# Performance work log

Measured on AMD Instinct MI355X. Metric: run time of the kernel, lower is better.

Reference implementation:

```python
import jax, jax.numpy as jnp
import numpy as np

D_MODEL = 1024
N_HEADS = 16
HEAD_DIM = D_MODEL // N_HEADS


def setup_inputs() -> dict:
    key = jax.random.key(0)
    ks = jax.random.split(key, 9)
    s = 1.0 / np.sqrt(D_MODEL)
    inp = {
        "x": jax.random.normal(ks[0], (4, 2048, D_MODEL), dtype=jnp.float32),
        "wq": jax.random.uniform(ks[1], (D_MODEL, D_MODEL), jnp.float32, -s, s),
        "bq": jax.random.uniform(ks[2], (D_MODEL,), jnp.float32, -s, s),
        "wk": jax.random.uniform(ks[3], (D_MODEL, D_MODEL), jnp.float32, -s, s),
        "bk": jax.random.uniform(ks[4], (D_MODEL,), jnp.float32, -s, s),
        "wv": jax.random.uniform(ks[5], (D_MODEL, D_MODEL), jnp.float32, -s, s),
        "bv": jax.random.uniform(ks[6], (D_MODEL,), jnp.float32, -s, s),
        "wo": jax.random.uniform(ks[7], (D_MODEL, D_MODEL), jnp.float32, -s, s),
        "bo": jax.random.uniform(ks[8], (D_MODEL,), jnp.float32, -s, s),
    }
    return inp


def reference(x, wq, bq, wk, bk, wv, bv, wo, bo):
    b, s, d = x.shape
    h, hd = N_HEADS, HEAD_DIM
    # projections (torch Linear: y = x @ W.T + b; here weights stored as [in, out])
    q = (x @ wq + bq).reshape(b, s, h, hd).transpose(0, 2, 1, 3)  # [b,h,s,hd]
    k = (x @ wk + bk).reshape(b, s, h, hd).transpose(0, 2, 1, 3)
    v = (x @ wv + bv).reshape(b, s, h, hd).transpose(0, 2, 1, 3)
    scores = jnp.einsum("bhqd,bhkd->bhqk", q, k) / jnp.sqrt(jnp.float32(hd))
    causal = jnp.tril(jnp.ones((s, s), dtype=bool))
    scores = jnp.where(causal, scores, -jnp.inf)
    weights = jax.nn.softmax(scores, axis=-1)
    attn = jnp.einsum("bhqk,bhkd->bhqd", weights, v)  # [b,h,s,hd]
    attn = attn.transpose(0, 2, 1, 3).reshape(b, s, d)
    return attn @ wo + bo
```

## Files before the change

kernel.cpp:

```cpp
#include <hip/hip_runtime.h>
#include <cstddef>

#define D_MODEL 1024
#define NH 16
#define HD 64
#define BATCH 4
#define SEQ 2048
#define MTOT (BATCH * SEQ)

typedef _Float16 half8 __attribute__((ext_vector_type(8)));
typedef _Float16 half4v __attribute__((ext_vector_type(4)));
typedef float f32x4 __attribute__((ext_vector_type(4)));

#if __has_builtin(__builtin_amdgcn_exp2f)
#define EXP2(x) __builtin_amdgcn_exp2f(x)
#else
#define EXP2(x) __expf((x)*0.69314718056f)
#endif

__global__ __launch_bounds__(256) void prep(
    const float* __restrict__ x, _Float16* __restrict__ xh,
    const float* __restrict__ W0, const float* __restrict__ W1,
    const float* __restrict__ W2, const float* __restrict__ W3,
    _Float16* __restrict__ T0, _Float16* __restrict__ T1,
    _Float16* __restrict__ T2, _Float16* __restrict__ T3)
{
    __shared__ float T[64][65];
    const int bid = blockIdx.x;
    if (bid < 256) {
        const size_t base = (size_t)bid * 4096 + threadIdx.x;
#pragma unroll
        for (int it = 0; it < 16; ++it) {
            const size_t i = base + (size_t)it * 256;
            const float4* p = (const float4*)x + 2 * i;
            float4 a = p[0], b = p[1];
            half8 h;
            h[0] = (_Float16)a.x; h[1] = (_Float16)a.y; h[2] = (_Float16)a.z; h[3] = (_Float16)a.w;
            h[4] = (_Float16)b.x; h[5] = (_Float16)b.y; h[6] = (_Float16)b.z; h[7] = (_Float16)b.w;
            *((half8*)xh + i) = h;
        }
    } else {
        const int t = bid - 256;
        const int mtx = t >> 8;
        const float* W = (mtx == 0) ? W0 : (mtx == 1) ? W1 : (mtx == 2) ? W2 : W3;
        _Float16*   Wt = (mtx == 0) ? T0 : (mtx == 1) ? T1 : (mtx == 2) ? T2 : T3;
        const int tile = t & 255;
        const int k0 = (tile >> 4) * 64, n0 = (tile & 15) * 64;
        const int r = threadIdx.x >> 4, c4 = (threadIdx.x & 15) * 4;

#pragma unroll
        for (int i = 0; i < 4; ++i) {
            float4 v = *(const float4*)(W + (size_t)(k0 + r + 16 * i) * 1024 + n0 + c4);
            T[r + 16 * i][c4 + 0] = v.x; T[r + 16 * i][c4 + 1] = v.y;
            T[r + 16 * i][c4 + 2] = v.z; T[r + 16 * i][c4 + 3] = v.w;
        }
        __syncthreads();
#pragma unroll
        for (int i = 0; i < 4; ++i) {
            const int n = r + 16 * i;
            half4v h;
            h[0] = (_Float16)T[c4 + 0][n]; h[1] = (_Float16)T[c4 + 1][n];
            h[2] = (_Float16)T[c4 + 2][n]; h[3] = (_Float16)T[c4 + 3][n];
            *(half4v*)(Wt + (size_t)(n0 + n) * 1024 + k0 + c4) = h;
        }
    }
}

template <int QKV>
__global__ __launch_bounds__(256) void gemm_mfma(
    const _Float16* __restrict__ A,
    const _Float16* __restrict__ Bt0, const _Float16* __restrict__ Bt1, const _Float16* __restrict__ Bt2,
    const float* __restrict__ bi0, const float* __restrict__ bi1, const float* __restrict__ bi2,
    void* __restrict__ C0, void* __restrict__ C1, void* __restrict__ C2)
{
    const int L = blockIdx.x;
    const int y = L & 63;
    const int c_ = L >> 6;
    const int z  = QKV ? (c_ >> 3) : 0;
    const int xb = QKV ? (c_ & 7) : c_;

    const _Float16* Bt = (z == 0) ? Bt0 : (z == 1) ? Bt1 : Bt2;
    const float*   bia = (z == 0) ? bi0 : (z == 1) ? bi1 : bi2;
    void*            C = (z == 0) ? C0  : (z == 1) ? C1  : C2;

    __shared__ _Float16 As[128][72];
    __shared__ _Float16 Bs[128][72];

    const int tid  = threadIdx.x;
    const int w    = tid >> 6;
    const int lane = tid & 63;
    const int l15  = lane & 15;
    const int lg   = lane >> 4;
    const int m0 = y * 128;
    const int n0 = xb * 128;
    const int wm = (w >> 1) * 64, wn = (w & 1) * 64;

    const int srow = tid >> 3;
    const int scol = (tid & 7) * 8;

    const _Float16* Ab = A + (size_t)(m0 + srow) * 1024 + scol;
    const _Float16* Bb = Bt + (size_t)(n0 + srow) * 1024 + scol;

    half8 aR[4], bR[4];
#pragma unroll
    for (int i = 0; i < 4; ++i) {
        aR[i] = *(const half8*)(Ab + (size_t)(32 * i) * 1024);
        bR[i] = *(const half8*)(Bb + (size_t)(32 * i) * 1024);
    }

    f32x4 acc[4][4];
#pragma unroll
    for (int i = 0; i < 4; ++i)
#pragma unroll
        for (int j = 0; j < 4; ++j) { acc[i][j][0] = 0.f; acc[i][j][1] = 0.f; acc[i][j][2] = 0.f; acc[i][j][3] = 0.f; }

    for (int kt = 0; kt < 16; ++kt) {
        __syncthreads();
#pragma unroll
        for (int i = 0; i < 4; ++i) {
            *(half8*)&As[srow + 32 * i][scol] = aR[i];
            *(half8*)&Bs[srow + 32 * i][scol] = bR[i];
        }
        __syncthreads();
        if (kt < 15) {
            const int k0 = (kt + 1) * 64;
#pragma unroll
            for (int i = 0; i < 4; ++i) {
                aR[i] = *(const half8*)(Ab + (size_t)(32 * i) * 1024 + k0);
                bR[i] = *(const half8*)(Bb + (size_t)(32 * i) * 1024 + k0);
            }
        }
#pragma unroll
        for (int c = 0; c < 2; ++c) {
            half8 af[4], bf[4];
#pragma unroll
            for (int i = 0; i < 4; ++i) af[i] = *(const half8*)&As[wm + 16 * i + l15][32 * c + 8 * lg];
#pragma unroll
            for (int j = 0; j < 4; ++j) bf[j] = *(const half8*)&Bs[wn + 16 * j + l15][32 * c + 8 * lg];
#pragma unroll
            for (int i = 0; i < 4; ++i)
#pragma unroll
                for (int j = 0; j < 4; ++j)
                    acc[i][j] = __builtin_amdgcn_mfma_f32_16x16x32_f16(af[i], bf[j], acc[i][j], 0, 0, 0);
        }
    }

    float bv[4];
#pragma unroll
    for (int j = 0; j < 4; ++j) bv[j] = bia[n0 + wn + 16 * j + l15];

#pragma unroll
    for (int i = 0; i < 4; ++i)
#pragma unroll
        for (int j = 0; j < 4; ++j)
#pragma unroll
            for (int r = 0; r < 4; ++r) {
                const int m = m0 + wm + 16 * i + 4 * lg + r;
                const int n = n0 + wn + 16 * j + l15;
                const float val = acc[i][j][r] + bv[j];
                if (QKV) {
                    const int bb = m >> 11, ss = m & 2047, hh = n >> 6, hd = n & 63;
                    if (z < 2)
                        ((_Float16*)C)[((size_t)(bb * NH + hh) * SEQ + ss) * HD + hd] = (_Float16)val;
                    else
                        ((_Float16*)C)[((size_t)(bb * NH + hh) * HD + hd) * SEQ + ss] = (_Float16)val;
                } else {
                    ((float*)C)[(size_t)m * 1024 + n] = val;
                }
            }
}

__global__ __launch_bounds__(256, 4) void attn_fwd_mfma(
    const _Float16* __restrict__ Q, const _Float16* __restrict__ K,
    const _Float16* __restrict__ Vt, _Float16* __restrict__ O)
{
    __shared__ _Float16 Ks[64][80];
    __shared__ _Float16 Vs[64][80];
    __shared__ _Float16 Ps[4][16][80];

    const int tid  = threadIdx.x;
    const int w    = tid >> 6;
    const int lane = tid & 63;
    const int l15  = lane & 15;
    const int lg   = lane >> 4;

    const int bh = blockIdx.y;
    const int b  = bh >> 4, h = bh & 15;

    const _Float16* Qb  = Q  + (size_t)bh * SEQ * HD;
    const _Float16* Kb  = K  + (size_t)bh * SEQ * HD;
    const _Float16* Vtb = Vt + (size_t)bh * HD * SEQ;

    const int srow = tid >> 3;
    const int scol = (tid & 7) * 8;

    for (int pass = 0; pass < 2; ++pass) {
        const int qt = pass ? (int)blockIdx.x : (31 - (int)blockIdx.x);
        const int q0 = qt * 64;
        const int ntiles = qt + 1;

        half8 qa[2];
        {
            const _Float16* qp = Qb + (size_t)(q0 + 16 * w + l15) * HD + 8 * lg;
            qa[0] = *(const half8*)(qp);
            qa[1] = *(const half8*)(qp + 32);
#pragma unroll
            for (int c = 0; c < 2; ++c)
#pragma unroll
                for (int j = 0; j < 8; ++j)
                    qa[c][j] = (_Float16)((float)qa[c][j] * 0.18033688f);
        }

        f32x4 o_[4];
#pragma unroll
        for (int ft = 0; ft < 4; ++ft) { o_[ft][0] = 0.f; o_[ft][1] = 0.f; o_[ft][2] = 0.f; o_[ft][3] = 0.f; }
        float lp[4] = {0.f, 0.f, 0.f, 0.f};

        half8 kreg[2], vreg[2];
#pragma unroll
        for (int j = 0; j < 2; ++j) {
            kreg[j] = *(const half8*)(Kb  + (size_t)(srow + 32 * j) * HD + scol);
            vreg[j] = *(const half8*)(Vtb + (size_t)(srow + 32 * j) * SEQ + scol);
        }

        for (int kt = 0; kt < ntiles; ++kt) {
            __syncthreads();
#pragma unroll
            for (int j = 0; j < 2; ++j) {
                *(half8*)&Ks[srow + 32 * j][scol] = kreg[j];
                *(half8*)&Vs[srow + 32 * j][scol] = vreg[j];
            }
            __syncthreads();

            if (kt + 1 < ntiles) {
                const int k0 = (kt + 1) * 64;
#pragma unroll
                for (int j = 0; j < 2; ++j) {
                    kreg[j] = *(const half8*)(Kb  + (size_t)(k0 + srow + 32 * j) * HD + scol);
                    vreg[j] = *(const half8*)(Vtb + (size_t)(srow + 32 * j) * SEQ + k0 + scol);
                }
            }

            f32x4 s[4];
#pragma unroll
            for (int f = 0; f < 4; ++f) { s[f][0] = 0.f; s[f][1] = 0.f; s[f][2] = 0.f; s[f][3] = 0.f; }
#pragma unroll
            for (int c = 0; c < 2; ++c)
#pragma unroll
                for (int f = 0; f < 4; ++f) {
                    half8 kb = *(const half8*)&Ks[16 * f + l15][32 * c + 8 * lg];
                    s[f] = __builtin_amdgcn_mfma_f32_16x16x32_f16(qa[c], kb, s[f], 0, 0, 0);
                }

            const bool dg = (kt == qt);
#pragma unroll
            for (int f = 0; f < 4; ++f)
#pragma unroll
                for (int r = 0; r < 4; ++r) {
                    float p = EXP2(s[f][r]);
                    if (dg && (16 * f + l15 > 16 * w + 4 * lg + r)) p = 0.f;
                    lp[r] += p;
                    Ps[w][4 * lg + r][16 * f + l15] = (_Float16)p;
                }

            half8 pa[2];
            pa[0] = *(const half8*)&Ps[w][l15][8 * lg];
            pa[1] = *(const half8*)&Ps[w][l15][32 + 8 * lg];
#pragma unroll
            for (int c = 0; c < 2; ++c)
#pragma unroll
                for (int ft = 0; ft < 4; ++ft) {
                    half8 vb = *(const half8*)&Vs[16 * ft + l15][32 * c + 8 * lg];
                    o_[ft] = __builtin_amdgcn_mfma_f32_16x16x32_f16(pa[c], vb, o_[ft], 0, 0, 0);
                }
        }

#pragma unroll
        for (int r = 0; r < 4; ++r) {
            float rs = lp[r];
            rs += __shfl_xor(rs, 1);
            rs += __shfl_xor(rs, 2);
            rs += __shfl_xor(rs, 4);
            rs += __shfl_xor(rs, 8);
            const float inv = 1.0f / rs;
            _Float16* orow = O + (size_t)(b * SEQ + q0 + 16 * w + 4 * lg + r) * D_MODEL + h * HD + l15;
#pragma unroll
            for (int ft = 0; ft < 4; ++ft) orow[16 * ft] = (_Float16)(o_[ft][r] * inv);
        }
        __syncthreads();
    }
}

extern "C" void kernel_launch(void* const* d_in, const int* in_sizes, int n_in,
                              void* d_out, int out_size, void* d_ws, size_t ws_size,
                              hipStream_t stream)
{
    const float* x  = (const float*)d_in[0];
    const float* wq = (const float*)d_in[1];
    const float* bq = (const float*)d_in[2];
    const float* wk = (const float*)d_in[3];
    const float* bk = (const float*)d_in[4];
    const float* wv = (const float*)d_in[5];
    const float* bv = (const float*)d_in[6];
    const float* wo = (const float*)d_in[7];
    const float* bo = (const float*)d_in[8];
    float* out = (float*)d_out;

    const size_t SZ = (size_t)MTOT * D_MODEL;
    const size_t WZ = (size_t)D_MODEL * D_MODEL;

    _Float16* xh  = (_Float16*)d_ws;
    _Float16* wtq = xh + SZ;
    _Float16* wtk = wtq + WZ;
    _Float16* wtv = wtk + WZ;
    _Float16* wto = wtv + WZ;
    _Float16* Qh  = wto + WZ;
    _Float16* Kh  = Qh + SZ;
    _Float16* Vtg = Kh + SZ;
    _Float16* AOh = Vtg + SZ;

    prep<<<dim3(1280), 256, 0, stream>>>(x, xh, wq, wk, wv, wo, wtq, wtk, wtv, wto);
    gemm_mfma<1><<<dim3(1536), 256, 0, stream>>>(xh, wtq, wtk, wtv, bq, bk, bv, Qh, Kh, Vtg);
    attn_fwd_mfma<<<dim3(16, BATCH * NH), 256, 0, stream>>>(Qh, Kh, Vtg, AOh);
    gemm_mfma<0><<<dim3(512), 256, 0, stream>>>(AOh, wto, wto, wto, bo, bo, bo, out, out, out);
}
```

Measured before the change: 272.1 us.

## Load A operands directly from global memory into registers, share only B tile

```diff
diff --git a/kernel.cpp b/kernel.cpp
--- a/kernel.cpp
+++ b/kernel.cpp
@@ -66,104 +66,108 @@
     }
 }
 
-template <int QKV>
-__global__ __launch_bounds__(256) void gemm_mfma(
+template <int QKV, int BMW>
+__global__ __launch_bounds__(256, (BMW == 64) ? 3 : 4) void gemm_flat(
     const _Float16* __restrict__ A,
     const _Float16* __restrict__ Bt0, const _Float16* __restrict__ Bt1, const _Float16* __restrict__ Bt2,
     const float* __restrict__ bi0, const float* __restrict__ bi1, const float* __restrict__ bi2,
     void* __restrict__ C0, void* __restrict__ C1, void* __restrict__ C2)
 {
-    const int L = blockIdx.x;
-    const int y = L & 63;
-    const int c_ = L >> 6;
-    const int z  = QKV ? (c_ >> 3) : 0;
-    const int xb = QKV ? (c_ & 7) : c_;
+    constexpr int NI = BMW / 16;
+    constexpr int MB = QKV ? 32 : 64;
+
+    const int L  = blockIdx.x;
+    const int y  = L & (MB - 1);
+    const int c_ = L / MB;
+    const int z  = QKV ? (c_ >> 4) : 0;
+    const int xb = QKV ? (c_ & 15) : c_;
 
     const _Float16* Bt = (z == 0) ? Bt0 : (z == 1) ? Bt1 : Bt2;
     const float*   bia = (z == 0) ? bi0 : (z == 1) ? bi1 : bi2;
     void*            C = (z == 0) ? C0  : (z == 1) ? C1  : C2;
 
-    __shared__ _Float16 As[128][72];
-    __shared__ _Float16 Bs[128][72];
+    __shared__ _Float16 Bs[64][72];
 
     const int tid  = threadIdx.x;
     const int w    = tid >> 6;
     const int lane = tid & 63;
     const int l15  = lane & 15;
     const int lg   = lane >> 4;
-    const int m0 = y * 128;
-    const int n0 = xb * 128;
-    const int wm = (w >> 1) * 64, wn = (w & 1) * 64;
+    const int m0 = y * (4 * BMW);
+    const int n0 = xb * 64;
 
     const int srow = tid >> 3;
     const int scol = (tid & 7) * 8;
 
-    const _Float16* Ab = A + (size_t)(m0 + srow) * 1024 + scol;
     const _Float16* Bb = Bt + (size_t)(n0 + srow) * 1024 + scol;
-
-    half8 aR[4], bR[4];
-#pragma unroll
-    for (int i = 0; i < 4; ++i) {
-        aR[i] = *(const half8*)(Ab + (size_t)(32 * i) * 1024);
-        bR[i] = *(const half8*)(Bb + (size_t)(32 * i) * 1024);
-    }
-
-    f32x4 acc[4][4];
-#pragma unroll
-    for (int i = 0; i < 4; ++i)
+    const _Float16* Aw = A + (size_t)(m0 + w * BMW + l15) * 1024 + 8 * lg;
+
+    half8 bR[2];
+#pragma unroll
+    for (int j = 0; j < 2; ++j)
+        bR[j] = *(const half8*)(Bb + (size_t)(32 * j) * 1024);
+
+    f32x4 acc[NI][4];
+#pragma unroll
+    for (int i = 0; i < NI; ++i)
 #pragma unroll
         for (int j = 0; j < 4; ++j) { acc[i][j][0] = 0.f; acc[i][j][1] = 0.f; acc[i][j][2] = 0.f; acc[i][j][3] = 0.f; }
 
     for (int kt = 0; kt < 16; ++kt) {
+        const int k0 = kt * 64;
         __syncthreads();
 #pragma unroll
-        for (int i = 0; i < 4; ++i) {
-            *(half8*)&As[srow + 32 * i][scol] = aR[i];
-            *(half8*)&Bs[srow + 32 * i][scol] = bR[i];
-        }
+        for (int j = 0; j < 2; ++j)
+            *(half8*)&Bs[srow + 32 * j][scol] = bR[j];
         __syncthreads();
         if (kt < 15) {
-            const int k0 = (kt + 1) * 64;
-#pragma unroll
-            for (int i = 0; i < 4; ++i) {
-                aR[i] = *(const half8*)(Ab + (size_t)(32 * i) * 1024 + k0);
-                bR[i] = *(const half8*)(Bb + (size_t)(32 * i) * 1024 + k0);
-            }
-        }
-#pragma unroll
-        for (int c = 0; c < 2; ++c) {
-            half8 af[4], bf[4];
-#pragma unroll
-            for (int i = 0; i < 4; ++i) af[i] = *(const half8*)&As[wm + 16 * i + l15][32 * c + 8 * lg];
-#pragma unroll
-            for (int j = 0; j < 4; ++j) bf[j] = *(const half8*)&Bs[wn + 16 * j + l15][32 * c + 8 * lg];
-#pragma unroll
-            for (int i = 0; i < 4; ++i)
+#pragma unroll
+            for (int j = 0; j < 2; ++j)
+                bR[j] = *(const half8*)(Bb + (size_t)(32 * j) * 1024 + k0 + 64);
+        }
+
+        half8 af[NI][2];
+#pragma unroll
+        for (int i = 0; i < NI; ++i)
+#pragma unroll
+            for (int c = 0; c < 2; ++c)
+                af[i][c] = *(const half8*)(Aw + (size_t)(16 * i) * 1024 + k0 + 32 * c);
+
+        half8 bf[4][2];
+#pragma unroll
+        for (int j = 0; j < 4; ++j)
+#pragma unroll
+            for (int c = 0; c < 2; ++c)
+                bf[j][c] = *(const half8*)&Bs[16 * j + l15][32 * c + 8 * lg];
+
+#pragma unroll
+        for (int c = 0; c < 2; ++c)
+#pragma unroll
+            for (int i = 0; i < NI; ++i)
 #pragma unroll
                 for (int j = 0; j < 4; ++j)
-                    acc[i][j] = __builtin_amdgcn_mfma_f32_16x16x32_f16(af[i], bf[j], acc[i][j], 0, 0, 0);
-        }
+                    acc[i][j] = __builtin_amdgcn_mfma_f32_16x16x32_f16(af[i][c], bf[j][c], acc[i][j], 0, 0, 0);
     }
 
     float bv[4];
 #pragma unroll
-    for (int j = 0; j < 4; ++j) bv[j] = bia[n0 + wn + 16 * j + l15];
-
-#pragma unroll
-    for (int i = 0; i < 4; ++i)
+    for (int j = 0; j < 4; ++j) bv[j] = bia[n0 + 16 * j + l15];
+
+#pragma unroll
+    for (int i = 0; i < NI; ++i)
 #pragma unroll
         for (int j = 0; j < 4; ++j)
 #pragma unroll
             for (int r = 0; r < 4; ++r) {
-                const int m = m0 + wm + 16 * i + 4 * lg + r;
-                const int n = n0 + wn + 16 * j + l15;
+                const int m = m0 + w * BMW + 16 * i + 4 * lg + r;
+                const int n = n0 + 16 * j + l15;
                 const float val = acc[i][j][r] + bv[j];
                 if (QKV) {
-                    const int bb = m >> 11, ss = m & 2047, hh = n >> 6, hd = n & 63;
+                    const int bb = m >> 11, ss = m & 2047, hd = n & 63;
                     if (z < 2)
-                        ((_Float16*)C)[((size_t)(bb * NH + hh) * SEQ + ss) * HD + hd] = (_Float16)val;
+                        ((_Float16*)C)[((size_t)(bb * NH + xb) * SEQ + ss) * HD + hd] = (_Float16)val;
                     else
-                        ((_Float16*)C)[((size_t)(bb * NH + hh) * HD + hd) * SEQ + ss] = (_Float16)val;
+                        ((_Float16*)C)[((size_t)(bb * NH + xb) * HD + hd) * SEQ + ss] = (_Float16)val;
                 } else {
                     ((float*)C)[(size_t)m * 1024 + n] = val;
                 }
@@ -320,7 +324,7 @@
     _Float16* AOh = Vtg + SZ;
 
     prep<<<dim3(1280), 256, 0, stream>>>(x, xh, wq, wk, wv, wo, wtq, wtk, wtv, wto);
-    gemm_mfma<1><<<dim3(1536), 256, 0, stream>>>(xh, wtq, wtk, wtv, bq, bk, bv, Qh, Kh, Vtg);
+    gemm_flat<1, 64><<<dim3(1536), 256, 0, stream>>>(xh, wtq, wtk, wtv, bq, bk, bv, Qh, Kh, Vtg);
     attn_fwd_mfma<<<dim3(16, BATCH * NH), 256, 0, stream>>>(Qh, Kh, Vtg, AOh);
-    gemm_mfma<0><<<dim3(512), 256, 0, stream>>>(AOh, wto, wto, wto, bo, bo, bo, out, out, out);
+    gemm_flat<0, 32><<<dim3(1024), 256, 0, stream>>>(AOh, wto, wto, wto, bo, bo, bo, out, out, out);
 }
```

Result: slower. 324.3 us (+19.2%).
